# Kernel optimization log

Hardware: AMD Instinct MI355X
Metric: run time of the kernel (lower is better)

The kernel has to match this reference:

```python
import jax, jax.numpy as jnp
import numpy as np

B, C, D, H = 1024, 119, 1024, 16
DH = D // H  # head dim = 64
EPS = 1e-5


def setup_inputs() -> dict:
    key = jax.random.key(0)
    ks = jax.random.split(key, 16)
    s = lambda n: 1.0 / np.sqrt(n)
    return {
        "board_tensor": jax.random.normal(ks[0], (B, C, 8, 8), jnp.float32),
        "emb_W": jax.random.normal(ks[1], (C, D), jnp.float32) * s(C),
        "emb_b": jnp.zeros((D,), jnp.float32),
        "positional": jnp.zeros((1, 64, D), jnp.float32),
        "Wq": jax.random.normal(ks[2], (D, D), jnp.float32) * s(D),
        "bq": jnp.zeros((D,), jnp.float32),
        "Wk": jax.random.normal(ks[3], (D, D), jnp.float32) * s(D),
        "bk": jnp.zeros((D,), jnp.float32),
        "Wv": jax.random.normal(ks[4], (D, D), jnp.float32) * s(D),
        "bv": jnp.zeros((D,), jnp.float32),
        "Wo": jax.random.normal(ks[5], (D, D), jnp.float32) * s(D),
        "bo": jnp.zeros((D,), jnp.float32),
        "rel_bias": jax.random.normal(ks[6], (H, 64, 64), jnp.float32) * 0.02,
        "ln_g": jnp.ones((D,), jnp.float32),
        "ln_b": jnp.zeros((D,), jnp.float32),
    }


def _layernorm(x, g, b):
    mu = jnp.mean(x, axis=-1, keepdims=True)
    var = jnp.mean(jnp.square(x - mu), axis=-1, keepdims=True)
    return (x - mu) * jax.lax.rsqrt(var + EPS) * g + b


def reference(board_tensor, emb_W, emb_b, positional, Wq, bq, Wk, bk, Wv, bv,
              Wo, bo, rel_bias, ln_g, ln_b):
    b = board_tensor.shape[0]
    # (B, C, 8, 8) -> (B, 64, C)
    x = board_tensor.reshape(b, C, 64).transpose(0, 2, 1)
    x = x @ emb_W + emb_b            # embedding GEMM -> (B, 64, D)
    x = x + positional
    # chess relative attention with learned per-head 64x64 bias
    q = (x @ Wq + bq).reshape(b, 64, H, DH)
    k = (x @ Wk + bk).reshape(b, 64, H, DH)
    v = (x @ Wv + bv).reshape(b, 64, H, DH)
    scores = jnp.einsum('bqhd,bkhd->bhqk', q, k) / np.sqrt(DH) + rel_bias
    attn = jax.nn.softmax(scores, axis=-1)
    o = jnp.einsum('bhqk,bkhd->bqhd', attn, v).reshape(b, 64, D)
    o = o @ Wo + bo
    # residual + LayerNorm
    return _layernorm(x + o, ln_g, ln_b)
```

## Files before the change

### kernel.cpp

```cpp
#include <hip/hip_runtime.h>
#include <hip/hip_bf16.h>
#include <stdint.h>


typedef float  floatx4 __attribute__((ext_vector_type(4)));
typedef short  bf16x8  __attribute__((ext_vector_type(8)));
typedef short  bf16x4  __attribute__((ext_vector_type(4)));

__device__ __forceinline__ short f2bf(float f) {
  __hip_bfloat16 h = __float2bfloat16(f);
  return *reinterpret_cast<short*>(&h);
}
__device__ __forceinline__ float bf2f(short s) {
  union { float f; uint32_t u; } c;
  c.u = ((uint32_t)(uint16_t)s) << 16;
  return c.f;
}
__device__ __forceinline__ floatx4 mfma16(bf16x8 a, bf16x8 b, floatx4 c) {
  return __builtin_amdgcn_mfma_f32_16x16x32_bf16(a, b, c, 0, 0, 0);
}

#define ASYNC_CP16(gsrc, ldst)                                                 \
  __builtin_amdgcn_global_load_lds(                                            \
      (const __attribute__((address_space(1))) void*)(gsrc),                   \
      (__attribute__((address_space(3))) void*)(ldst), 16, 0, 0)

__global__ void k_transpose4(const float* __restrict__ Wq,
                             const float* __restrict__ Wk,
                             const float* __restrict__ Wv,
                             const float* __restrict__ Wo,
                             short* __restrict__ dstBase) {
  __shared__ float tile[32][33];
  const int z = blockIdx.z;
  const float* src = (z == 0) ? Wq : (z == 1) ? Wk : (z == 2) ? Wv : Wo;
  short* dst = dstBase + (size_t)z * 1024 * 1024;
  const int bx = blockIdx.x * 32, by = blockIdx.y * 32;
  const int tx = threadIdx.x, ty = threadIdx.y;
#pragma unroll
  for (int i = 0; i < 32; i += 8)
    tile[ty + i][tx] = src[(size_t)(by + ty + i) * 1024 + bx + tx];
  __syncthreads();
#pragma unroll
  for (int i = 0; i < 32; i += 8)
    dst[(size_t)(bx + ty + i) * 1024 + by + tx] = f2bf(tile[tx][ty + i]);
}

__global__ void k_embWt(const float* __restrict__ embW, short* __restrict__ dst) {
  const int idx = blockIdx.x * 256 + threadIdx.x;
  const int n = idx >> 7, c = idx & 127;
  dst[idx] = f2bf((c < 119) ? embW[(size_t)c * 1024 + n] : 0.f);
}

__global__ __launch_bounds__(256) void k_embed(
    const float* __restrict__ board, const short* __restrict__ embWt,
    const float* __restrict__ emb_b, const float* __restrict__ pos,
    short* __restrict__ x) {
  __shared__ short As[64 * 136];
  __shared__ short Bs[128 * 32];
  const int t = threadIdx.x, l = t & 63, w = t >> 6;
  const int quad = l >> 4, lan = l & 15;
  const int xcd = blockIdx.x & 7;
  const int lin = (blockIdx.x >> 3) + xcd * 1024;
  const int b = lin >> 3, nBase = (lin & 7) << 7;
  const float* bb = board + (size_t)b * (119 * 64);
  const int s = t & 63;
#pragma unroll
  for (int it = 0; it < 16; ++it) {
    const int c0 = ((t >> 6) + it * 4) * 2;
    float u0 = (c0 < 119) ? bb[c0 * 64 + s] : 0.f;
    float u1 = (c0 + 1 < 119) ? bb[(c0 + 1) * 64 + s] : 0.f;
    short2 pr; pr.x = f2bf(u0); pr.y = f2bf(u1);
    *(short2*)&As[s * 136 + c0] = pr;
  }
  const short* Bg0 = embWt + (size_t)(nBase + (t >> 2)) * 128 + (t & 3) * 8;
  const short* Bg1 = Bg0 + (size_t)64 * 128;
  short* Bs0 = &Bs[(w * 16) * 32];
  short* Bs1 = &Bs[(64 + w * 16) * 32];
  floatx4 acc[4][2] = {};
  __syncthreads();
  for (int kk = 0; kk < 4; ++kk) {
    ASYNC_CP16(Bg0 + kk * 32, Bs0);
    ASYNC_CP16(Bg1 + kk * 32, Bs1);
    __syncthreads();
    bf16x8 af[4], bfr[2];
#pragma unroll
    for (int mt = 0; mt < 4; ++mt)
      af[mt] = *(const bf16x8*)&As[(mt * 16 + lan) * 136 + kk * 32 + quad * 8];
#pragma unroll
    for (int n2 = 0; n2 < 2; ++n2)
      bfr[n2] = *(const bf16x8*)&Bs[(w * 32 + n2 * 16 + lan) * 32 + quad * 8];
#pragma unroll
    for (int mt = 0; mt < 4; ++mt)
#pragma unroll
      for (int n2 = 0; n2 < 2; ++n2)
        acc[mt][n2] = mfma16(af[mt], bfr[n2], acc[mt][n2]);
    __syncthreads();
  }
#pragma unroll
  for (int n2 = 0; n2 < 2; ++n2) {
    const int n = nBase + w * 32 + n2 * 16 + lan;
    const float bi = emb_b[n];
#pragma unroll
    for (int mt = 0; mt < 4; ++mt) {
      const int s0 = mt * 16 + quad * 4;
      floatx4 v = acc[mt][n2];
#pragma unroll
      for (int r = 0; r < 4; ++r) {
        const int ss = s0 + r;
        x[((size_t)b * 64 + ss) * 1024 + n] = f2bf(v[r] + bi + pos[ss * 1024 + n]);
      }
    }
  }
}

__device__ __forceinline__ void gemm8_core(
    const short* __restrict__ A, const short* __restrict__ Bt,
    short* lds, const int mBase, const int nBase, floatx4 (&acc)[8][4]) {
  const int t = threadIdx.x;
  const int w = t >> 6, l = t & 63;
  const int lan = l & 15, quad = l >> 4;
  const int wm = w >> 2, wn = w & 3;
  const int row0 = t >> 2;
  const int sg = (t & 3) ^ ((t >> 3) & 3);
  const short* Ag = A + (size_t)(mBase + row0) * 1024 + sg * 8;
  const short* Bg = Bt + (size_t)(nBase + row0) * 1024 + sg * 8;
  const int swz = (quad ^ ((lan >> 1) & 3)) * 8;
  const int aRd = (wm * 128 + lan) * 32 + swz;
  const int bRd = 32768 + (wn * 64 + lan) * 32 + swz;
  const int wst = w * 512;

#define STAGE_A8(ktgt, kh, buf) do {                                          \
    const short* _s = Ag + (ktgt) * 64 + (kh) * 32;                           \
    ASYNC_CP16(_s,          &lds[(buf) * 16384 + (kh) * 8192 + wst]);          \
    ASYNC_CP16(_s + 131072, &lds[(buf) * 16384 + (kh) * 8192 + 4096 + wst]);   \
  } while (0)
#define STAGE_B8(ktgt, kh, buf) do {                                          \
    const short* _s = Bg + (ktgt) * 64 + (kh) * 32;                           \
    ASYNC_CP16(_s,          &lds[32768 + (buf) * 16384 + (kh) * 8192 + wst]);  \
    ASYNC_CP16(_s + 131072,                                                    \
               &lds[32768 + (buf) * 16384 + (kh) * 8192 + 4096 + wst]);        \
  } while (0)
#define LDA8(dst, buf, ks, mh)                                                \
    _Pragma("unroll") for (int mf = 0; mf < 4; ++mf)                          \
      dst[mf] = *(const bf16x8*)&lds[(buf) * 16384 + (ks) * 8192 + aRd +      \
                                     ((mh) * 64 + mf * 16) * 32];
#define LDB8(dst, buf, ks)                                                    \
    _Pragma("unroll") for (int nf = 0; nf < 4; ++nf)                          \
      dst[nf] = *(const bf16x8*)&lds[(buf) * 16384 + (ks) * 8192 + bRd +      \
                                     nf * 512];
#define MMA8(mh, bfr)                                                         \
    _Pragma("unroll") for (int mf = 0; mf < 4; ++mf)                          \
      _Pragma("unroll") for (int nf = 0; nf < 4; ++nf)                        \
        acc[(mh) * 4 + mf][nf] = mfma16(af[mf], bfr[nf], acc[(mh) * 4 + mf][nf]);
#define PHASE_MID                                                             \
    __builtin_amdgcn_sched_barrier(0);                                        \
    __builtin_amdgcn_s_barrier();                                             \
    asm volatile("s_waitcnt lgkmcnt(0)" ::: "memory");                        \
    __builtin_amdgcn_sched_barrier(0);                                        \
    __builtin_amdgcn_s_setprio(1)
#define PHASE_END                                                             \
    __builtin_amdgcn_s_setprio(0);                                            \
    __builtin_amdgcn_sched_barrier(0);                                        \
    __builtin_amdgcn_s_barrier()
#define PHASE_END_VM                                                          \
    __builtin_amdgcn_s_setprio(0);                                            \
    __builtin_amdgcn_sched_barrier(0);                                        \
    asm volatile("s_waitcnt vmcnt(4)" ::: "memory");                          \
    __builtin_amdgcn_s_barrier()

  STAGE_A8(0, 0, 0); STAGE_B8(0, 0, 0);
  STAGE_A8(0, 1, 0); STAGE_B8(0, 1, 0);
  STAGE_A8(1, 0, 1); STAGE_B8(1, 0, 1);
  asm volatile("s_waitcnt vmcnt(4)" ::: "memory");
  __builtin_amdgcn_sched_barrier(0);
  __builtin_amdgcn_s_barrier();

#define TILE8(kt, cur) do {                                                   \
    const int k1 = ((kt) + 1 < 16) ? (kt) + 1 : 15;                           \
    const int k2 = ((kt) + 2 < 16) ? (kt) + 2 : 15;                           \
    bf16x8 af[4], bf0[4], bf1[4];                                             \
                                                          \
    LDA8(af, cur, 0, 0); LDB8(bf0, cur, 0);                                   \
    STAGE_A8(k1, 1, (cur) ^ 1);                                               \
    PHASE_MID; MMA8(0, bf0); PHASE_END;                                       \
                                                          \
    LDA8(af, cur, 0, 1);                                                      \
    STAGE_B8(k1, 1, (cur) ^ 1);                                               \
    PHASE_MID; MMA8(1, bf0); PHASE_END;                                       \
                                                          \
    LDA8(af, cur, 1, 0); LDB8(bf1, cur, 1);                                   \
    STAGE_A8(k2, 0, cur);                                                     \
    PHASE_MID; MMA8(0, bf1); PHASE_END;                                       \
                           \
    LDA8(af, cur, 1, 1);                                                      \
    STAGE_B8(k2, 0, cur);                                                     \
    PHASE_MID; MMA8(1, bf1); PHASE_END_VM;                                    \
  } while (0)

#pragma unroll 1
  for (int it = 0; it < 8; ++it) {
    TILE8(it * 2, 0);
    TILE8(it * 2 + 1, 1);
  }
  asm volatile("s_waitcnt vmcnt(0)" ::: "memory");
#undef TILE8
#undef PHASE_END_VM
#undef PHASE_END
#undef PHASE_MID
#undef MMA8
#undef LDB8
#undef LDA8
#undef STAGE_B8
#undef STAGE_A8
}

__global__ __launch_bounds__(512, 2) void k_gemm_qkv8(
    const short* __restrict__ A, const short* __restrict__ Bt,
    const float* __restrict__ bq, const float* __restrict__ bk,
    const float* __restrict__ bv, short* __restrict__ qb,
    short* __restrict__ kb, short* __restrict__ vtb) {
  __shared__ short lds[65536];
  const int xcd = blockIdx.x & 7;
  const int lin = (blockIdx.x >> 3) + xcd * 384;
  const int grp = lin / 96;
  const int rem = lin - grp * 96;
  const int mBase = ((grp << 3) + (rem & 7)) << 8;
  const int nBase = (rem >> 3) << 8;

  floatx4 acc[8][4] = {};
  gemm8_core(A, Bt, lds, mBase, nBase, acc);

  const int t = threadIdx.x, w = t >> 6, l = t & 63;
  const int lan = l & 15, quad = l >> 4;
  const int wm = w >> 2, wn = w & 3;
  const int region = nBase >> 10;
  const int nb = nBase & 1023;
  const float* bias = (region == 0) ? bq : (region == 1) ? bk : bv;
  short* qk = (region == 0) ? qb : kb;
#pragma unroll
  for (int am = 0; am < 8; ++am) {
    const int m0 = mBase + wm * 128 + am * 16 + quad * 4;
    const int b = m0 >> 6, s0 = m0 & 63;
#pragma unroll
    for (int nf = 0; nf < 4; ++nf) {
      const int nn = nb + wn * 64 + nf * 16 + lan;
      const int h = nn >> 6, dh = nn & 63;
      const float bi = bias[nn];
      floatx4 v = acc[am][nf];
      if (region < 2) {
        short* dst = qk + (((size_t)b * 16 + h) * 64 + s0) * 64 + dh;
        dst[0]   = f2bf(v.x + bi);
        dst[64]  = f2bf(v.y + bi);
        dst[128] = f2bf(v.z + bi);
        dst[192] = f2bf(v.w + bi);
      } else {
        bf16x4 pk = {f2bf(v.x + bi), f2bf(v.y + bi), f2bf(v.z + bi), f2bf(v.w + bi)};
        *(bf16x4*)(vtb + (((size_t)b * 16 + h) * 64 + dh) * 64 + s0) = pk;
      }
    }
  }
}

__global__ __launch_bounds__(512, 2) void k_gemm_oproj8(
    const short* __restrict__ A, const short* __restrict__ Bt,
    const float* __restrict__ bo, const short* __restrict__ xres,
    short* __restrict__ y) {
  __shared__ short lds[65536];
  const int xcd = blockIdx.x & 7;
  const int lin = (blockIdx.x >> 3) + xcd * 128;
  const int grp = lin >> 5;
  const int rem = lin & 31;
  const int mBase = ((grp << 3) + (rem & 7)) << 8;
  const int nBase = (rem >> 3) << 8;

  floatx4 acc[8][4] = {};
  gemm8_core(A, Bt, lds, mBase, nBase, acc);

  const int t = threadIdx.x, w = t >> 6, l = t & 63;
  const int lan = l & 15, quad = l >> 4;
  const int wm = w >> 2, wn = w & 3;
#pragma unroll
  for (int nf = 0; nf < 4; ++nf) {
    const int n = nBase + wn * 64 + nf * 16 + lan;
    const float bi = bo[n];
#pragma unroll
    for (int am = 0; am < 8; ++am) {
      const int m0 = mBase + wm * 128 + am * 16 + quad * 4;
      floatx4 v = acc[am][nf];
#pragma unroll
      for (int r = 0; r < 4; ++r) {
        const size_t idx = (size_t)(m0 + r) * 1024 + n;
        y[idx] = f2bf(v[r] + bi + bf2f(xres[idx]));
      }
    }
  }
}

__global__ __launch_bounds__(256) void k_attn(
    const short* __restrict__ qb, const short* __restrict__ kb,
    const short* __restrict__ vtb, const float* __restrict__ rel_bias,
    short* __restrict__ ob) {
  __shared__ short P[4][64 * 72];
  const int t = threadIdx.x, l = t & 63, w = t >> 6;
  const int quad = l >> 4, lan = l & 15;
  const int b = blockIdx.x >> 2;
  const int h = (blockIdx.x & 3) * 4 + w;
  const short* q  = qb  + ((size_t)b * 16 + h) * 4096;
  const short* kp = kb  + ((size_t)b * 16 + h) * 4096;
  const short* vt = vtb + ((size_t)b * 16 + h) * 4096;
  const float* bias = rel_bias + (size_t)h * 4096;
  short* Pw = &P[w][0];

  bf16x8 kf[4][2], qf[4][2];
#pragma unroll
  for (int mt = 0; mt < 4; ++mt) {
    kf[mt][0] = *(const bf16x8*)&kp[(mt * 16 + lan) * 64 + quad * 8];
    kf[mt][1] = *(const bf16x8*)&kp[(mt * 16 + lan) * 64 + 32 + quad * 8];
  }
#pragma unroll
  for (int nt = 0; nt < 4; ++nt) {
    qf[nt][0] = *(const bf16x8*)&q[(nt * 16 + lan) * 64 + quad * 8];
    qf[nt][1] = *(const bf16x8*)&q[(nt * 16 + lan) * 64 + 32 + quad * 8];
  }
  floatx4 S[4][4];
#pragma unroll
  for (int mt = 0; mt < 4; ++mt)
#pragma unroll
    for (int nt = 0; nt < 4; ++nt) {
      floatx4 z = {0.f, 0.f, 0.f, 0.f};
      z = mfma16(kf[mt][0], qf[nt][0], z);
      S[mt][nt] = mfma16(kf[mt][1], qf[nt][1], z);
    }
  float rs[4];
#pragma unroll
  for (int nt = 0; nt < 4; ++nt) {
    const int qi = nt * 16 + lan;
    float sv[4][4];
    float m = -1e30f;
#pragma unroll
    for (int mt = 0; mt < 4; ++mt) {
      floatx4 bi = *(const floatx4*)&bias[qi * 64 + mt * 16 + quad * 4];
#pragma unroll
      for (int r = 0; r < 4; ++r) {
        sv[mt][r] = fmaf(S[mt][nt][r], 0.125f, bi[r]);
        m = fmaxf(m, sv[mt][r]);
      }
    }
    m = fmaxf(m, __shfl_xor(m, 16));
    m = fmaxf(m, __shfl_xor(m, 32));
    float sum = 0.f;
#pragma unroll
    for (int mt = 0; mt < 4; ++mt) {
      float p0 = exp2f((sv[mt][0] - m) * 1.4426950408889634f);
      float p1 = exp2f((sv[mt][1] - m) * 1.4426950408889634f);
      float p2 = exp2f((sv[mt][2] - m) * 1.4426950408889634f);
      float p3 = exp2f((sv[mt][3] - m) * 1.4426950408889634f);
      sum += p0 + p1 + p2 + p3;
      bf16x4 pk = {f2bf(p0), f2bf(p1), f2bf(p2), f2bf(p3)};
      *(bf16x4*)&Pw[qi * 72 + mt * 16 + quad * 4] = pk;
    }
    sum += __shfl_xor(sum, 16);
    sum += __shfl_xor(sum, 32);
    rs[nt] = 1.0f / sum;
  }
  bf16x8 pf[4][2];
#pragma unroll
  for (int nt = 0; nt < 4; ++nt) {
    pf[nt][0] = *(const bf16x8*)&Pw[(nt * 16 + lan) * 72 + quad * 8];
    pf[nt][1] = *(const bf16x8*)&Pw[(nt * 16 + lan) * 72 + 32 + quad * 8];
  }
#pragma unroll
  for (int mo = 0; mo < 4; ++mo) {
    bf16x8 vf0 = *(const bf16x8*)&vt[(mo * 16 + lan) * 64 + quad * 8];
    bf16x8 vf1 = *(const bf16x8*)&vt[(mo * 16 + lan) * 64 + 32 + quad * 8];
#pragma unroll
    for (int nt = 0; nt < 4; ++nt) {
      floatx4 z = {0.f, 0.f, 0.f, 0.f};
      z = mfma16(vf0, pf[nt][0], z);
      z = mfma16(vf1, pf[nt][1], z);
      const int qi = nt * 16 + lan;
      const int dh0 = mo * 16 + quad * 4;
      const float r = rs[nt];
      bf16x4 pk = {f2bf(z.x * r), f2bf(z.y * r), f2bf(z.z * r), f2bf(z.w * r)};
      *(bf16x4*)&ob[((size_t)b * 64 + qi) * 1024 + h * 64 + dh0] = pk;
    }
  }
}

__global__ __launch_bounds__(256) void k_ln2(
    const short* __restrict__ y, const float* __restrict__ g,
    const float* __restrict__ be, float* __restrict__ out) {
  const int t = threadIdx.x, w = t >> 6, lane = t & 63;
#pragma unroll
  for (int it = 0; it < 4; ++it) {
    const int row = blockIdx.x * 16 + it * 4 + w;
    const short* yr = y + (size_t)row * 1024 + lane * 16;
    bf16x8 a = *(const bf16x8*)yr;
    bf16x8 c = *(const bf16x8*)(yr + 8);
    float v[16];
#pragma unroll
    for (int j = 0; j < 8; ++j) { v[j] = bf2f(a[j]); v[8 + j] = bf2f(c[j]); }
    float s = 0.f, s2 = 0.f;
#pragma unroll
    for (int j = 0; j < 16; ++j) { s += v[j]; s2 += v[j] * v[j]; }
#pragma unroll
    for (int off = 1; off < 64; off <<= 1) {
      s  += __shfl_xor(s, off);
      s2 += __shfl_xor(s2, off);
    }
    const float mu = s * (1.f / 1024.f);
    const float var = s2 * (1.f / 1024.f) - mu * mu;
    const float rstd = rsqrtf(var + 1e-5f);
    const int c0 = lane * 16;
    float* op = out + (size_t)row * 1024 + c0;
#pragma unroll
    for (int j4 = 0; j4 < 4; ++j4) {
      float4 gg = *(const float4*)&g[c0 + j4 * 4];
      float4 bb = *(const float4*)&be[c0 + j4 * 4];
      float4 o;
      o.x = (v[j4 * 4 + 0] - mu) * rstd * gg.x + bb.x;
      o.y = (v[j4 * 4 + 1] - mu) * rstd * gg.y + bb.y;
      o.z = (v[j4 * 4 + 2] - mu) * rstd * gg.z + bb.z;
      o.w = (v[j4 * 4 + 3] - mu) * rstd * gg.w + bb.w;
      *(float4*)&op[j4 * 4] = o;
    }
  }
}

extern "C" void kernel_launch(void* const* d_in, const int* in_sizes, int n_in,
                              void* d_out, int out_size, void* d_ws,
                              size_t ws_size, hipStream_t stream) {
  const float* board    = (const float*)d_in[0];
  const float* emb_W    = (const float*)d_in[1];
  const float* emb_b    = (const float*)d_in[2];
  const float* pos      = (const float*)d_in[3];
  const float* Wq       = (const float*)d_in[4];
  const float* bq       = (const float*)d_in[5];
  const float* Wk       = (const float*)d_in[6];
  const float* bk       = (const float*)d_in[7];
  const float* Wv       = (const float*)d_in[8];
  const float* bv       = (const float*)d_in[9];
  const float* Wo       = (const float*)d_in[10];
  const float* bo       = (const float*)d_in[11];
  const float* rel_bias = (const float*)d_in[12];
  const float* ln_g     = (const float*)d_in[13];
  const float* ln_b     = (const float*)d_in[14];

  char* ws = (char*)d_ws;
  short* Wqkv_t = (short*)ws; ws += (size_t)3072 * 1024 * 2;
  short* Wo_t   = (short*)ws; ws += (size_t)1024 * 1024 * 2;
  short* embWt  = (short*)ws; ws += (size_t)1024 * 128 * 2;
  short* xb     = (short*)ws; ws += (size_t)65536 * 1024 * 2;
  short* qb     = (short*)ws; ws += (size_t)16384 * 4096 * 2;
  short* kb     = (short*)ws; ws += (size_t)16384 * 4096 * 2;
  short* vtb    = (short*)ws; ws += (size_t)16384 * 4096 * 2;
  short* ob     = (short*)ws; ws += (size_t)65536 * 1024 * 2;
  short* yb     = kb;

  k_transpose4<<<dim3(32, 32, 4), dim3(32, 8), 0, stream>>>(Wq, Wk, Wv, Wo,
                                                            Wqkv_t);
  k_embWt<<<512, 256, 0, stream>>>(emb_W, embWt);

  k_embed<<<8192, 256, 0, stream>>>(board, embWt, emb_b, pos, xb);
  k_gemm_qkv8<<<3072, 512, 0, stream>>>(xb, Wqkv_t, bq, bk, bv, qb, kb, vtb);
  k_attn<<<4096, 256, 0, stream>>>(qb, kb, vtb, rel_bias, ob);
  k_gemm_oproj8<<<1024, 512, 0, stream>>>(ob, Wo_t, bo, xb, yb);
  k_ln2<<<4096, 256, 0, stream>>>(yb, ln_g, ln_b, (float*)d_out);
}
```

Measured before the change: 1.356 ms.

## Use 128x128 tile GEMM core with higher occupancy for output projection

Adds a new GEMM core that computes 128x128 output tiles with eight waves, each holding a 32x64 sub-tile, using a smaller LDS footprint and a finer-grained double-buffered async staging schedule. The output projection switches to this core with four times as many blocks and a launch bound allowing four blocks per CU. This aims to improve occupancy and latency hiding for the projection GEMM. The cost is lower data reuse per tile, so more global and LDS traffic per FLOP.

```diff
diff --git a/kernel.cpp b/kernel.cpp
--- a/kernel.cpp
+++ b/kernel.cpp
@@ -179,19 +179,15 @@
     const int k1 = ((kt) + 1 < 16) ? (kt) + 1 : 15;                           \
     const int k2 = ((kt) + 2 < 16) ? (kt) + 2 : 15;                           \
     bf16x8 af[4], bf0[4], bf1[4];                                             \
-                                                          \
     LDA8(af, cur, 0, 0); LDB8(bf0, cur, 0);                                   \
     STAGE_A8(k1, 1, (cur) ^ 1);                                               \
     PHASE_MID; MMA8(0, bf0); PHASE_END;                                       \
-                                                          \
     LDA8(af, cur, 0, 1);                                                      \
     STAGE_B8(k1, 1, (cur) ^ 1);                                               \
     PHASE_MID; MMA8(1, bf0); PHASE_END;                                       \
-                                                          \
     LDA8(af, cur, 1, 0); LDB8(bf1, cur, 1);                                   \
     STAGE_A8(k2, 0, cur);                                                     \
     PHASE_MID; MMA8(0, bf1); PHASE_END;                                       \
-                           \
     LDA8(af, cur, 1, 1);                                                      \
     STAGE_B8(k2, 0, cur);                                                     \
     PHASE_MID; MMA8(1, bf1); PHASE_END_VM;                                    \
@@ -212,6 +208,75 @@
 #undef LDA8
 #undef STAGE_B8
 #undef STAGE_A8
+}
+
+__device__ __forceinline__ void gemm128_core(
+    const short* __restrict__ A, const short* __restrict__ Bt,
+    short* lds, const int mBase, const int nBase, floatx4 (&acc)[2][4]) {
+  const int t = threadIdx.x;
+  const int w = t >> 6, l = t & 63;
+  const int lan = l & 15, quad = l >> 4;
+  const int wm = w >> 1, wn = w & 1;
+  const int srow = t >> 2;
+  const int sg = ((t & 3) ^ ((t >> 3) & 3)) * 8;
+  const short* Ag = A + (size_t)(mBase + srow) * 1024 + sg;
+  const short* Bg = Bt + (size_t)(nBase + srow) * 1024 + sg;
+  const int swz = (quad ^ ((lan >> 1) & 3)) * 8;
+  const int aRd = (wm * 32 + lan) * 32 + swz;
+  const int bRd = 8192 + (wn * 64 + lan) * 32 + swz;
+  const int wst = w * 512;
+
+#define STAGE_AB(ko, kh, buf) do {                                            \
+    ASYNC_CP16(Ag + (ko) + (kh) * 32,                                         \
+               &lds[(buf) * 16384 + (kh) * 4096 + wst]);                       \
+    ASYNC_CP16(Bg + (ko) + (kh) * 32,                                         \
+               &lds[8192 + (buf) * 16384 + (kh) * 4096 + wst]);                \
+  } while (0)
+
+#define PHASE(buf, kh, stko, stkh, stbuf) do {                                \
+    bf16x8 af[2], bfr[4];                                                     \
+    _Pragma("unroll") for (int am = 0; am < 2; ++am)                          \
+      af[am] = *(const bf16x8*)&lds[(buf) * 16384 + (kh) * 4096 + aRd +       \
+                                    am * 512];                                 \
+    _Pragma("unroll") for (int nf = 0; nf < 4; ++nf)                          \
+      bfr[nf] = *(const bf16x8*)&lds[(buf) * 16384 + (kh) * 4096 + bRd +      \
+                                     nf * 512];                                \
+    STAGE_AB(stko, stkh, stbuf);                                              \
+    __builtin_amdgcn_sched_barrier(0);                                        \
+    __builtin_amdgcn_s_barrier();                                             \
+    asm volatile("s_waitcnt lgkmcnt(0)" ::: "memory");                        \
+    __builtin_amdgcn_sched_barrier(0);                                        \
+    __builtin_amdgcn_s_setprio(1);                                            \
+    _Pragma("unroll") for (int am = 0; am < 2; ++am)                          \
+      _Pragma("unroll") for (int nf = 0; nf < 4; ++nf)                        \
+        acc[am][nf] = mfma16(af[am], bfr[nf], acc[am][nf]);                   \
+    __builtin_amdgcn_s_setprio(0);                                            \
+    __builtin_amdgcn_sched_barrier(0);                                        \
+    asm volatile("s_waitcnt vmcnt(4)" ::: "memory");                          \
+    __builtin_amdgcn_s_barrier();                                             \
+  } while (0)
+
+  STAGE_AB(0, 0, 0);
+  STAGE_AB(0, 1, 0);
+  STAGE_AB(64, 0, 1);
+  asm volatile("s_waitcnt vmcnt(4)" ::: "memory");
+  __builtin_amdgcn_sched_barrier(0);
+  __builtin_amdgcn_s_barrier();
+
+#pragma unroll 1
+  for (int tt = 0; tt < 16; tt += 2) {
+    const int k1 = (tt + 1) * 64;
+    const int k2 = (tt + 2 < 16 ? tt + 2 : 15) * 64;
+    const int k3 = (tt + 3 < 16 ? tt + 3 : 15) * 64;
+    PHASE(0, 0, k1, 1, 1);
+    PHASE(0, 1, k2, 0, 0);
+    PHASE(1, 0, k2, 1, 0);
+    PHASE(1, 1, k3, 0, 1);
+  }
+  asm volatile("s_waitcnt vmcnt(0)" ::: "memory");
+  __builtin_amdgcn_s_barrier();
+#undef PHASE
+#undef STAGE_AB
 }
 
 __global__ __launch_bounds__(512, 2) void k_gemm_qkv8(
@@ -261,31 +326,31 @@
   }
 }
 
-__global__ __launch_bounds__(512, 2) void k_gemm_oproj8(
+__global__ __launch_bounds__(512, 4) void k_gemm_oproj10(
     const short* __restrict__ A, const short* __restrict__ Bt,
     const float* __restrict__ bo, const short* __restrict__ xres,
     short* __restrict__ y) {
-  __shared__ short lds[65536];
+  __shared__ short lds[32768];
   const int xcd = blockIdx.x & 7;
-  const int lin = (blockIdx.x >> 3) + xcd * 128;
-  const int grp = lin >> 5;
-  const int rem = lin & 31;
-  const int mBase = ((grp << 3) + (rem & 7)) << 8;
-  const int nBase = (rem >> 3) << 8;
-
-  floatx4 acc[8][4] = {};
-  gemm8_core(A, Bt, lds, mBase, nBase, acc);
+  const int lin = (blockIdx.x >> 3) + xcd * 512;
+  const int grp = lin >> 6;
+  const int rem = lin & 63;
+  const int mBase = ((grp << 3) + (rem & 7)) << 7;
+  const int nBase = (rem >> 3) << 7;
+
+  floatx4 acc[2][4] = {};
+  gemm128_core(A, Bt, lds, mBase, nBase, acc);
 
   const int t = threadIdx.x, w = t >> 6, l = t & 63;
   const int lan = l & 15, quad = l >> 4;
-  const int wm = w >> 2, wn = w & 3;
+  const int wm = w >> 1, wn = w & 1;
 #pragma unroll
   for (int nf = 0; nf < 4; ++nf) {
     const int n = nBase + wn * 64 + nf * 16 + lan;
     const float bi = bo[n];
 #pragma unroll
-    for (int am = 0; am < 8; ++am) {
-      const int m0 = mBase + wm * 128 + am * 16 + quad * 4;
+    for (int am = 0; am < 2; ++am) {
+      const int m0 = mBase + wm * 32 + am * 16 + quad * 4;
       floatx4 v = acc[am][nf];
 #pragma unroll
       for (int r = 0; r < 4; ++r) {
@@ -464,6 +529,6 @@
   k_embed<<<8192, 256, 0, stream>>>(board, embWt, emb_b, pos, xb);
   k_gemm_qkv8<<<3072, 512, 0, stream>>>(xb, Wqkv_t, bq, bk, bv, qb, kb, vtb);
   k_attn<<<4096, 256, 0, stream>>>(qb, kb, vtb, rel_bias, ob);
-  k_gemm_oproj8<<<1024, 512, 0, stream>>>(ob, Wo_t, bo, xb, yb);
+  k_gemm_oproj10<<<4096, 512, 0, stream>>>(ob, Wo_t, bo, xb, yb);
   k_ln2<<<4096, 256, 0, stream>>>(yb, ln_g, ln_b, (float*)d_out);
 }
```

After: 1.246 ms. -8.1%, faster.
